# Performance work log

Hardware: AMD Instinct MI355X
Metric: run time of the kernel (lower is better)

The kernel has to match this reference:

```python
import jax, jax.numpy as jnp
import numpy as np

D_MODEL = 1024
N_HEADS = 16
N_KV = 4
HEAD_DIM = 64
R = 256
B, N = 2, 2048


def setup_inputs() -> dict:
    key = jax.random.key(0)
    ks = jax.random.split(key, 5)
    x = jax.random.normal(ks[0], (B, N, D_MODEL), jnp.float32)
    # rotary cos/sin table: (N, HEAD_DIM//2, 2)
    inv = 1.0 / (10000.0 ** (jnp.arange(0, HEAD_DIM, 2, dtype=jnp.float32) / HEAD_DIM))
    ang = jnp.arange(N, dtype=jnp.float32)[:, None] * inv[None, :]
    freqs_cis = jnp.stack([jnp.cos(ang), jnp.sin(ang)], axis=-1)
    s = 0.02
    Wq = jax.random.normal(ks[1], (D_MODEL, N_HEADS * HEAD_DIM), jnp.float32) * s
    Wk = jax.random.normal(ks[2], (D_MODEL, N_KV * HEAD_DIM), jnp.float32) * s
    Wv = jax.random.normal(ks[3], (D_MODEL, N_KV * HEAD_DIM), jnp.float32) * s
    Wo = jax.random.normal(ks[4], (N_HEADS * HEAD_DIM, D_MODEL), jnp.float32) * s
    return dict(x=x, freqs_cis=freqs_cis, Wq=Wq, Wk=Wk, Wv=Wv, Wo=Wo)


def _select_pairs(scores_i, best_b_i, r):
    """Greedy top-r pair selection with unique-b constraint (one batch row)."""
    half = scores_i.shape[0]
    order = jnp.argsort(-scores_i)  # descending by best similarity

    def step(carry, a_local):
        used, count = carry
        b_local = best_b_i[a_local]
        take = jnp.logical_and(jnp.logical_not(used[b_local]), count < r)
        used = used.at[b_local].set(used[b_local] | take)
        count = count + take.astype(jnp.int32)
        return (used, count), (take, a_local.astype(jnp.int32), b_local.astype(jnp.int32))

    (_, count), (takes, a_locs, b_locs) = jax.lax.scan(
        step, (jnp.zeros(half, bool), jnp.int32(0)), order)
    pos = jnp.cumsum(takes.astype(jnp.int32)) - 1
    idx = jnp.where(takes, pos, r)  # dump non-taken into slot r
    sel_a = jnp.zeros(r + 1, jnp.int32).at[idx].set(a_locs)[:r]
    sel_b = jnp.zeros(r + 1, jnp.int32).at[idx].set(b_locs)[:r]
    valid = jnp.arange(r) < count  # pad (if fewer than r unique) with first pair
    sel_a = jnp.where(valid, sel_a, sel_a[0])
    sel_b = jnp.where(valid, sel_b, sel_b[0])
    return sel_a, sel_b


def bipartite_indices(metric, r):
    """Returns (global_a, global_b, keep_idx) for merge/unmerge."""
    Bm, Nm, _ = metric.shape
    a = metric[:, 0::2]  # (B, half, C)
    b = metric[:, 1::2]
    an = a / jnp.maximum(jnp.linalg.norm(a, axis=-1, keepdims=True), 1e-12)
    bn = b / jnp.maximum(jnp.linalg.norm(b, axis=-1, keepdims=True), 1e-12)
    scores = jnp.einsum('bic,bjc->bij', an, bn)  # (B, half, half)
    best_scores = scores.max(axis=2)
    best_b = scores.argmax(axis=2)
    sel_a, sel_b = jax.vmap(lambda s, m: _select_pairs(s, m, r))(best_scores, best_b)
    global_a = 2 * sel_a      # even indices
    global_b = 2 * sel_b + 1  # odd indices
    bidx = jnp.arange(Bm)[:, None]
    keep_mask = jnp.ones((Bm, Nm), bool).at[bidx, global_b].set(False)
    # stable argsort puts kept (False) positions first, in original order
    keep_idx = jnp.argsort(~keep_mask, axis=1)[:, :Nm - r]
    return global_a, global_b, keep_idx


def merge(x, global_a, global_b, keep_idx):
    Bm = x.shape[0]
    bidx = jnp.arange(Bm)[:, None]
    xa = jnp.take_along_axis(x, global_a[..., None], axis=1)
    xb = jnp.take_along_axis(x, global_b[..., None], axis=1)
    x_out = x.at[bidx, global_a].set((xa + xb) * 0.5)
    return jnp.take_along_axis(x_out, keep_idx[..., None], axis=1)


def unmerge(xm, global_a, global_b, keep_idx, n_orig):
    Bm, _, C = xm.shape
    bidx = jnp.arange(Bm)[:, None]
    out = jnp.zeros((Bm, n_orig, C), xm.dtype).at[bidx, keep_idx].set(xm)
    xa = jnp.take_along_axis(out, global_a[..., None], axis=1)
    return out.at[bidx, global_b].set(xa)


def _rope(t, freqs):
    # t: (B, N, H, HD), freqs: (N, HD//2, 2)
    cos = freqs[None, :, None, :, 0]
    sin = freqs[None, :, None, :, 1]
    t1 = t[..., 0::2]
    t2 = t[..., 1::2]
    rot = jnp.stack([t1 * cos - t2 * sin, t1 * sin + t2 * cos], axis=-1)
    return rot.reshape(t.shape)


def _attention(x_m, freqs, Wq, Wk, Wv, Wo):
    Bm, Nm, _ = x_m.shape
    q = (x_m @ Wq).reshape(Bm, Nm, N_HEADS, HEAD_DIM)
    k = (x_m @ Wk).reshape(Bm, Nm, N_KV, HEAD_DIM)
    v = (x_m @ Wv).reshape(Bm, Nm, N_KV, HEAD_DIM)
    q = _rope(q, freqs)
    k = _rope(k, freqs)
    rep = N_HEADS // N_KV
    k = jnp.repeat(k, rep, axis=2)
    v = jnp.repeat(v, rep, axis=2)
    att = jnp.einsum('bqhd,bkhd->bhqk', q, k) / np.sqrt(HEAD_DIM).astype(np.float32)
    w = jax.nn.softmax(att, axis=-1)
    o = jnp.einsum('bhqk,bkhd->bqhd', w, v).reshape(Bm, Nm, N_HEADS * HEAD_DIM)
    return o @ Wo


def reference(x, freqs_cis, Wq, Wk, Wv, Wo):
    n = x.shape[1]
    metric = jax.lax.stop_gradient(x @ Wk)  # k_proj under no_grad
    ga, gb, ki = bipartite_indices(metric, R)
    x_m = merge(x, ga, gb, ki)
    n_merged = x_m.shape[1]
    out_m = _attention(x_m, freqs_cis[:n_merged], Wq, Wk, Wv, Wo)
    return unmerge(out_m, ga, gb, ki, n)
```

## Files before the change

kernel.cpp:

```cpp
#include <hip/hip_runtime.h>
#include <hip/hip_bf16.h>
#include <math.h>

#define BB 2
#define NN 2048
#define DM 1024
#define NH 16
#define NKV 4
#define HD 64
#define RR 256
#define HALF 1024
#define NM 1792
#define NT 28
#define NSPL 2

typedef __bf16 bf16x8 __attribute__((ext_vector_type(8)));
typedef float f32x4 __attribute__((ext_vector_type(4)));

__device__ inline unsigned pk2(float a, float b) {
  union { __bf16 h; unsigned short u; } ua, ub;
  ua.h = (__bf16)a;
  ub.h = (__bf16)b;
  return (unsigned)ua.u | ((unsigned)ub.u << 16);
}

__device__ inline unsigned shu(unsigned v, int s) {
  return (unsigned)__shfl((int)v, s, 64);
}

__global__ __launch_bounds__(256) void gemm_bf16(
    const __bf16* __restrict__ A, const __bf16* __restrict__ Bt,
    float* __restrict__ C, int M, int N, int K) {
  __shared__ __align__(16) __bf16 As[4096];
  __shared__ __align__(16) __bf16 Bs[4096];
  const int bm0 = blockIdx.x * 64;
  const int bn0 = blockIdx.y * 64;
  const int w = threadIdx.x >> 6;
  const int lane = threadIdx.x & 63;
  f32x4 acc[4];
#pragma unroll
  for (int nt = 0; nt < 4; ++nt) acc[nt] = (f32x4){0.f, 0.f, 0.f, 0.f};
  for (int kk = 0; kk < K; kk += 64) {
    __syncthreads();
#pragma unroll
    for (int t2 = threadIdx.x; t2 < 512; t2 += 256) {
      const int blk = t2 >> 7, s = (t2 >> 6) & 1, l = t2 & 63;
      const int kc = kk + s * 32 + ((l >> 4) << 3);
      *(float4*)&As[t2 * 8] =
          *(const float4*)(A + (size_t)(bm0 + blk * 16 + (l & 15)) * K + kc);
      *(float4*)&Bs[t2 * 8] =
          *(const float4*)(Bt + (size_t)(bn0 + blk * 16 + (l & 15)) * K + kc);
    }
    __syncthreads();
#pragma unroll
    for (int s = 0; s < 2; ++s) {
      bf16x8 a = *(const bf16x8*)&As[((w * 2 + s) * 64 + lane) * 8];
#pragma unroll
      for (int nt = 0; nt < 4; ++nt) {
        bf16x8 bfr = *(const bf16x8*)&Bs[((nt * 2 + s) * 64 + lane) * 8];
        acc[nt] =
            __builtin_amdgcn_mfma_f32_16x16x32_bf16(a, bfr, acc[nt], 0, 0, 0);
      }
    }
  }
  const int g = lane >> 4, ml = lane & 15;
#pragma unroll
  for (int nt = 0; nt < 4; ++nt)
#pragma unroll
    for (int r = 0; r < 4; ++r)
      C[(size_t)(bm0 + w * 16 + g * 4 + r) * N + bn0 + nt * 16 + ml] =
          acc[nt][r];
}

__global__ __launch_bounds__(256) void gemm_wo(
    const __bf16* __restrict__ A, const __bf16* __restrict__ Bt,
    const int* __restrict__ keep_idx, const int* __restrict__ dst2,
    float* __restrict__ out, int M, int N, int K) {
  __shared__ __align__(16) __bf16 As[4096];
  __shared__ __align__(16) __bf16 Bs[4096];
  const int bm0 = blockIdx.x * 64;
  const int bn0 = blockIdx.y * 64;
  const int w = threadIdx.x >> 6;
  const int lane = threadIdx.x & 63;
  f32x4 acc[4];
#pragma unroll
  for (int nt = 0; nt < 4; ++nt) acc[nt] = (f32x4){0.f, 0.f, 0.f, 0.f};
  for (int kk = 0; kk < K; kk += 64) {
    __syncthreads();
#pragma unroll
    for (int t2 = threadIdx.x; t2 < 512; t2 += 256) {
      const int blk = t2 >> 7, s = (t2 >> 6) & 1, l = t2 & 63;
      const int kc = kk + s * 32 + ((l >> 4) << 3);
      *(float4*)&As[t2 * 8] =
          *(const float4*)(A + (size_t)(bm0 + blk * 16 + (l & 15)) * K + kc);
      *(float4*)&Bs[t2 * 8] =
          *(const float4*)(Bt + (size_t)(bn0 + blk * 16 + (l & 15)) * K + kc);
    }
    __syncthreads();
#pragma unroll
    for (int s = 0; s < 2; ++s) {
      bf16x8 a = *(const bf16x8*)&As[((w * 2 + s) * 64 + lane) * 8];
#pragma unroll
      for (int nt = 0; nt < 4; ++nt) {
        bf16x8 bfr = *(const bf16x8*)&Bs[((nt * 2 + s) * 64 + lane) * 8];
        acc[nt] =
            __builtin_amdgcn_mfma_f32_16x16x32_bf16(a, bfr, acc[nt], 0, 0, 0);
      }
    }
  }
  const int g = lane >> 4, ml = lane & 15;
#pragma unroll
  for (int r = 0; r < 4; ++r) {
    const int row = bm0 + w * 16 + g * 4 + r;
    const int bb = row / NM, tt = row % NM;
    const int p1 = keep_idx[bb * NM + tt];
    const int p2 = dst2[bb * NM + tt];
#pragma unroll
    for (int nt = 0; nt < 4; ++nt) {
      const int col = bn0 + nt * 16 + ml;
      float v = acc[nt][r];
      out[((size_t)(bb * NN + p1)) * DM + col] = v;
      if (p2 >= 0) out[((size_t)(bb * NN + p2)) * DM + col] = v;
    }
  }
}

__global__ __launch_bounds__(256) void gemm_hiloA(
    const float* __restrict__ A, const __bf16* __restrict__ Bh,
    const __bf16* __restrict__ Bl, float* __restrict__ C0,
    float* __restrict__ C1, int M, int N, int K) {
  __shared__ __align__(16) __bf16 Ah[4096], Al[4096], Bhs[4096], Bls[4096];
  const int z = blockIdx.z;
  float* C = z ? C1 : C0;
  const int kof = z * (K / 2);
  const int bm0 = blockIdx.x * 64;
  const int bn0 = blockIdx.y * 64;
  const int w = threadIdx.x >> 6;
  const int lane = threadIdx.x & 63;
  f32x4 acc[4];
#pragma unroll
  for (int nt = 0; nt < 4; ++nt) acc[nt] = (f32x4){0.f, 0.f, 0.f, 0.f};
  for (int kk = kof; kk < kof + K / 2; kk += 64) {
    __syncthreads();
#pragma unroll
    for (int t2 = threadIdx.x; t2 < 512; t2 += 256) {
      const int blk = t2 >> 7, s = (t2 >> 6) & 1, l = t2 & 63;
      const int row = bm0 + blk * 16 + (l & 15);
      const int rowB = bn0 + blk * 16 + (l & 15);
      const int col = kk + s * 32 + ((l >> 4) << 3);
      {
        float4 f0 = *(const float4*)(A + (size_t)row * K + col);
        float4 f1 = *(const float4*)(A + (size_t)row * K + col + 4);
        float ff[8] = {f0.x, f0.y, f0.z, f0.w, f1.x, f1.y, f1.z, f1.w};
        union { __bf16 h[8]; float4 q; } H, L;
#pragma unroll
        for (int j = 0; j < 8; ++j) {
          __bf16 hh = (__bf16)ff[j];
          H.h[j] = hh;
          L.h[j] = (__bf16)(ff[j] - (float)hh);
        }
        *(float4*)&Ah[t2 * 8] = H.q;
        *(float4*)&Al[t2 * 8] = L.q;
      }
      *(float4*)&Bhs[t2 * 8] = *(const float4*)(Bh + (size_t)rowB * K + col);
      *(float4*)&Bls[t2 * 8] = *(const float4*)(Bl + (size_t)rowB * K + col);
    }
    __syncthreads();
#pragma unroll
    for (int s = 0; s < 2; ++s) {
      bf16x8 ah = *(const bf16x8*)&Ah[((w * 2 + s) * 64 + lane) * 8];
      bf16x8 al = *(const bf16x8*)&Al[((w * 2 + s) * 64 + lane) * 8];
#pragma unroll
      for (int nt = 0; nt < 4; ++nt) {
        bf16x8 bh = *(const bf16x8*)&Bhs[((nt * 2 + s) * 64 + lane) * 8];
        bf16x8 bl = *(const bf16x8*)&Bls[((nt * 2 + s) * 64 + lane) * 8];
        acc[nt] = __builtin_amdgcn_mfma_f32_16x16x32_bf16(al, bh, acc[nt], 0, 0, 0);
        acc[nt] = __builtin_amdgcn_mfma_f32_16x16x32_bf16(ah, bl, acc[nt], 0, 0, 0);
        acc[nt] = __builtin_amdgcn_mfma_f32_16x16x32_bf16(ah, bh, acc[nt], 0, 0, 0);
      }
    }
  }
  const int g = lane >> 4, ml = lane & 15;
#pragma unroll
  for (int nt = 0; nt < 4; ++nt)
#pragma unroll
    for (int r = 0; r < 4; ++r)
      C[(size_t)(bm0 + w * 16 + g * 4 + r) * N + bn0 + nt * 16 + ml] =
          acc[nt][r];
}

__global__ __launch_bounds__(256) void gemm_sc3(
    const __bf16* __restrict__ Ah, const __bf16* __restrict__ Al,
    const __bf16* __restrict__ Bh, const __bf16* __restrict__ Bl,
    float* __restrict__ C) {
  __shared__ __align__(16) __bf16 Ahs[4096], Als[4096], Bhs[4096], Bls[4096];
  const size_t zo = (size_t)blockIdx.z * HALF * 256;
  C += (size_t)blockIdx.z * HALF * HALF;
  const int bm0 = blockIdx.x * 64;
  const int bn0 = blockIdx.y * 64;
  const int w = threadIdx.x >> 6;
  const int lane = threadIdx.x & 63;
  f32x4 acc[4];
#pragma unroll
  for (int nt = 0; nt < 4; ++nt) acc[nt] = (f32x4){0.f, 0.f, 0.f, 0.f};
  for (int kk = 0; kk < 256; kk += 64) {
    __syncthreads();
#pragma unroll
    for (int t2 = threadIdx.x; t2 < 512; t2 += 256) {
      const int blk = t2 >> 7, s = (t2 >> 6) & 1, l = t2 & 63;
      const size_t ra = zo + (size_t)(bm0 + blk * 16 + (l & 15)) * 256;
      const size_t rb = zo + (size_t)(bn0 + blk * 16 + (l & 15)) * 256;
      const int col = kk + s * 32 + ((l >> 4) << 3);
      *(float4*)&Ahs[t2 * 8] = *(const float4*)(Ah + ra + col);
      *(float4*)&Als[t2 * 8] = *(const float4*)(Al + ra + col);
      *(float4*)&Bhs[t2 * 8] = *(const float4*)(Bh + rb + col);
      *(float4*)&Bls[t2 * 8] = *(const float4*)(Bl + rb + col);
    }
    __syncthreads();
#pragma unroll
    for (int s = 0; s < 2; ++s) {
      bf16x8 ah = *(const bf16x8*)&Ahs[((w * 2 + s) * 64 + lane) * 8];
      bf16x8 al = *(const bf16x8*)&Als[((w * 2 + s) * 64 + lane) * 8];
#pragma unroll
      for (int nt = 0; nt < 4; ++nt) {
        bf16x8 bh = *(const bf16x8*)&Bhs[((nt * 2 + s) * 64 + lane) * 8];
        bf16x8 bl = *(const bf16x8*)&Bls[((nt * 2 + s) * 64 + lane) * 8];
        acc[nt] = __builtin_amdgcn_mfma_f32_16x16x32_bf16(al, bh, acc[nt], 0, 0, 0);
        acc[nt] = __builtin_amdgcn_mfma_f32_16x16x32_bf16(ah, bl, acc[nt], 0, 0, 0);
        acc[nt] = __builtin_amdgcn_mfma_f32_16x16x32_bf16(ah, bh, acc[nt], 0, 0, 0);
      }
    }
  }
  const int g = lane >> 4, ml = lane & 15;
#pragma unroll
  for (int nt = 0; nt < 4; ++nt)
#pragma unroll
    for (int r = 0; r < 4; ++r)
      C[(size_t)(bm0 + w * 16 + g * 4 + r) * HALF + bn0 + nt * 16 + ml] =
          acc[nt][r];
}

__global__ __launch_bounds__(256) void transpose_wk(
    const float* __restrict__ W, __bf16* __restrict__ Wh,
    __bf16* __restrict__ Wl) {
  __shared__ float ld[64][65];
  const int k0 = blockIdx.x * 64, n0 = blockIdx.y * 64;
  for (int i = threadIdx.x; i < 1024; i += 256) {
    int r = i >> 4, c4 = i & 15;
    float4 v = *(const float4*)(W + (size_t)(k0 + r) * 256 + n0 + c4 * 4);
    ld[r][c4 * 4 + 0] = v.x;
    ld[r][c4 * 4 + 1] = v.y;
    ld[r][c4 * 4 + 2] = v.z;
    ld[r][c4 * 4 + 3] = v.w;
  }
  __syncthreads();
  for (int i = threadIdx.x; i < 4096; i += 256) {
    int n = i >> 6, k = i & 63;
    float v = ld[k][n];
    __bf16 hh = (__bf16)v;
    Wh[(size_t)(n0 + n) * 1024 + k0 + k] = hh;
    Wl[(size_t)(n0 + n) * 1024 + k0 + k] = (__bf16)(v - (float)hh);
  }
}

__global__ __launch_bounds__(256) void transpose_bf16(
    const float* __restrict__ W, __bf16* __restrict__ Wt, int K, int N) {
  __shared__ float ld[64][65];
  const int k0 = blockIdx.x * 64, n0 = blockIdx.y * 64;
  for (int i = threadIdx.x; i < 1024; i += 256) {
    int r = i >> 4, c4 = i & 15;
    float4 v = *(const float4*)(W + (size_t)(k0 + r) * N + n0 + c4 * 4);
    ld[r][c4 * 4 + 0] = v.x;
    ld[r][c4 * 4 + 1] = v.y;
    ld[r][c4 * 4 + 2] = v.z;
    ld[r][c4 * 4 + 3] = v.w;
  }
  __syncthreads();
  for (int i = threadIdx.x; i < 4096; i += 256) {
    int n = i >> 6, k = i & 63;
    Wt[(size_t)(n0 + n) * K + k0 + k] = (__bf16)ld[k][n];
  }
}

__global__ __launch_bounds__(256) void normalize_split(
    const float* __restrict__ m0, const float* __restrict__ m1,
    __bf16* __restrict__ anh, __bf16* __restrict__ anl,
    __bf16* __restrict__ bnh, __bf16* __restrict__ bnl) {
  const int row = blockIdx.x;
  const int b = row >> 11;
  const int r = row & 2047;
  const int t = threadIdx.x;
  float v = m0[(size_t)row * 256 + t] + m1[(size_t)row * 256 + t];
  float ss = v * v;
#pragma unroll
  for (int o = 32; o > 0; o >>= 1) ss += __shfl_xor(ss, o, 64);
  __shared__ float wsum[4];
  if ((t & 63) == 0) wsum[t >> 6] = ss;
  __syncthreads();
  float tot = wsum[0] + wsum[1] + wsum[2] + wsum[3];
  float inv = 1.f / fmaxf(sqrtf(tot), 1e-12f);
  float nv = v * inv;
  __bf16 hh = (__bf16)nv;
  __bf16 ll = (__bf16)(nv - (float)hh);
  size_t o = ((size_t)b * HALF + (r >> 1)) * 256 + t;
  if (r & 1) {
    bnh[o] = hh;
    bnl[o] = ll;
  } else {
    anh[o] = hh;
    anl[o] = ll;
  }
}

__global__ __launch_bounds__(256) void argmax_rows(
    const float* __restrict__ scores, float* __restrict__ best_s,
    int* __restrict__ best_b) {
  const int rid = blockIdx.x * 4 + (threadIdx.x >> 6);
  const int lane = threadIdx.x & 63;
  const float4* row = (const float4*)(scores + (size_t)rid * 1024);
  float bv = -3.4e38f;
  int bj = 0;
#pragma unroll
  for (int p = 0; p < 4; ++p) {
    float4 f = row[p * 64 + lane];
    int j0 = (p * 64 + lane) * 4;
    if (f.x > bv) { bv = f.x; bj = j0; }
    if (f.y > bv) { bv = f.y; bj = j0 + 1; }
    if (f.z > bv) { bv = f.z; bj = j0 + 2; }
    if (f.w > bv) { bv = f.w; bj = j0 + 3; }
  }
#pragma unroll
  for (int off = 1; off < 64; off <<= 1) {
    float vo = __shfl_xor(bv, off, 64);
    int jo = __shfl_xor(bj, off, 64);
    if (vo > bv || (vo == bv && jo < bj)) { bv = vo; bj = jo; }
  }
  if (lane == 0) {
    best_s[rid] = bv;
    best_b[rid] = bj;
  }
}

__global__ __launch_bounds__(512) void sort_desc(const float* __restrict__ best_s,
                                                 int* __restrict__ order) {
  const int b = blockIdx.x;
  __shared__ float sv[1024];
  __shared__ int si[1024];
  for (int i = threadIdx.x; i < 1024; i += 512) {
    sv[i] = best_s[b * HALF + i];
    si[i] = i;
  }
  __syncthreads();
  for (int k = 2; k <= 1024; k <<= 1) {
    for (int j = k >> 1; j > 0; j >>= 1) {
      for (int t = threadIdx.x; t < 1024; t += 512) {
        int ixj = t ^ j;
        if (ixj > t) {
          bool dir = ((t & k) == 0);
          float va = sv[t], vb = sv[ixj];
          int ia = si[t], ib = si[ixj];
          bool before = (vb > va) || (vb == va && ib < ia);
          if (before == dir) {
            sv[t] = vb; sv[ixj] = va;
            si[t] = ib; si[ixj] = ia;
          }
        }
      }
      __syncthreads();
    }
  }
  for (int i = threadIdx.x; i < 1024; i += 512) order[b * HALF + i] = si[i];
}

__global__ __launch_bounds__(256) void select_and_index(
    const int* __restrict__ best_b, const int* __restrict__ order,
    int* __restrict__ keep_idx, int* __restrict__ partner,
    int* __restrict__ dst2) {
  const int b = blockIdx.x;
  __shared__ int rankA[HALF];
  __shared__ int minrank[HALF];
  __shared__ int taken[HALF];
  __shared__ int sel_a[RR], sel_b[RR];
  __shared__ int removed[NN];
  __shared__ int src_row[NN];
  __shared__ int tsum[256];
  const int t = threadIdx.x;

  for (int i = t; i < HALF; i += 256) { minrank[i] = 0x7fffffff; taken[i] = 0; }
  for (int i = t; i < NN; i += 256) {
    removed[i] = 0;
    partner[b * NN + i] = -1;
  }
  for (int i = t; i < NM; i += 256) dst2[b * NM + i] = -1;
  __syncthreads();
  int ord[4];
#pragma unroll
  for (int q = 0; q < 4; ++q) {
    int step = t * 4 + q;
    ord[q] = order[b * HALF + step];
    rankA[ord[q]] = step;
  }
  __syncthreads();
#pragma unroll
  for (int q = 0; q < 4; ++q) {
    int a = t * 4 + q;
    atomicMin(&minrank[best_b[b * HALF + a]], rankA[a]);
  }
  __syncthreads();
  for (int i = t; i < HALF; i += 256) {
    int mr = minrank[i];
    if (mr != 0x7fffffff) taken[mr] = 1;
  }
  __syncthreads();
  int c[4];
  int mysum = 0;
#pragma unroll
  for (int q = 0; q < 4; ++q) { c[q] = taken[t * 4 + q]; mysum += c[q]; }
  tsum[t] = mysum;
  __syncthreads();
  for (int off = 1; off < 256; off <<= 1) {
    int v = (t >= off) ? tsum[t - off] : 0;
    __syncthreads();
    tsum[t] += v;
    __syncthreads();
  }
  int run = tsum[t] - mysum;
#pragma unroll
  for (int q = 0; q < 4; ++q) {
    if (c[q] && run < RR) {
      int a = ord[q];
      sel_a[run] = 2 * a;
      sel_b[run] = 2 * best_b[b * HALF + a] + 1;
    }
    run += c[q];
  }
  __syncthreads();
  const int cnt = min(tsum[255], RR);
  if (t >= cnt) { sel_a[t] = sel_a[0]; sel_b[t] = sel_b[0]; }
  __syncthreads();
  {
    int ga = sel_a[t], gb = sel_b[t];
    removed[gb] = 1;
    partner[b * NN + ga] = gb;
  }
  __syncthreads();
  int myc = 0;
#pragma unroll
  for (int q = 0; q < 8; ++q) myc += !removed[8 * t + q];
  tsum[t] = myc;
  __syncthreads();
  for (int off = 1; off < 256; off <<= 1) {
    int v = (t >= off) ? tsum[t - off] : 0;
    __syncthreads();
    tsum[t] += v;
    __syncthreads();
  }
  int pos = tsum[t] - myc;
#pragma unroll
  for (int q = 0; q < 8; ++q) {
    int p = 8 * t + q;
    int sr = -1;
    if (!removed[p]) {
      if (pos < NM) {
        keep_idx[b * NM + pos] = p;
        sr = pos;
      }
      ++pos;
    }
    src_row[p] = sr;
  }
  __syncthreads();
  {
    int sr = src_row[sel_a[t]];
    dst2[b * NM + sr] = sel_b[t];
  }
}

__global__ __launch_bounds__(256) void merge_kernel(
    const float* __restrict__ x, const int* __restrict__ keep_idx,
    const int* __restrict__ partner, __bf16* __restrict__ x_mb) {
  const int mrow = blockIdx.x;
  const int b = mrow / NM;
  const int t = mrow % NM;
  const int p = keep_idx[b * NM + t];
  const int pp = partner[b * NN + p];
  const float4* src =
      reinterpret_cast<const float4*>(x + ((size_t)b * NN + p) * DM);
  float4 val = src[threadIdx.x];
  if (pp >= 0) {
    const float4* s2 =
        reinterpret_cast<const float4*>(x + ((size_t)b * NN + pp) * DM);
    float4 v2 = s2[threadIdx.x];
    val.x = 0.5f * (val.x + v2.x);
    val.y = 0.5f * (val.y + v2.y);
    val.z = 0.5f * (val.z + v2.z);
    val.w = 0.5f * (val.w + v2.w);
  }
  union { __bf16 h[4]; uint2 u; } U;
  U.h[0] = (__bf16)val.x;
  U.h[1] = (__bf16)val.y;
  U.h[2] = (__bf16)val.z;
  U.h[3] = (__bf16)val.w;
  ((uint2*)(x_mb + (size_t)mrow * DM))[threadIdx.x] = U.u;
}

__global__ __launch_bounds__(256) void rope_fused(
    const float* __restrict__ qb, const float* __restrict__ kb,
    const float* __restrict__ fc, __bf16* __restrict__ qbh,
    __bf16* __restrict__ kbh) {
  const int row = blockIdx.x;
  const int t = row % NM;
  const int b = row / NM;
  for (int idx = threadIdx.x; idx < 640; idx += 256) {
    int u = idx & 31;
    float c = fc[(t * 32 + u) * 2];
    float s = fc[(t * 32 + u) * 2 + 1];
    if (idx < 512) {
      int h = idx >> 5;
      const float* p = qb + (size_t)row * DM + h * 64 + 2 * u;
      float x1 = p[0], x2 = p[1];
      __bf16* d = qbh + ((size_t)(b * NH + h) * NM + t) * 64 + 2 * u;
      d[0] = (__bf16)((x1 * c - x2 * s) * 0.125f);
      d[1] = (__bf16)((x1 * s + x2 * c) * 0.125f);
    } else {
      int h = (idx - 512) >> 5;
      const float* p = kb + (size_t)row * 256 + h * 64 + 2 * u;
      float x1 = p[0], x2 = p[1];
      __bf16* d = kbh + ((size_t)(b * NKV + h) * NM + t) * 64 + 2 * u;
      d[0] = (__bf16)(x1 * c - x2 * s);
      d[1] = (__bf16)(x1 * s + x2 * c);
    }
  }
}

__global__ __launch_bounds__(256) void v_repack(const float* __restrict__ vb,
                                                __bf16* __restrict__ vtb) {
  __shared__ float ld[64][65];
  int bid = blockIdx.x;
  const int kt = bid % (NM / 64); bid /= (NM / 64);
  const int kvh = bid % NKV;
  const int b = bid / NKV;
  const int j0 = kt * 64;
  for (int t2 = threadIdx.x; t2 < 1024; t2 += 256) {
    int key = t2 >> 4, c4 = t2 & 15;
    float4 v4 = *reinterpret_cast<const float4*>(
        vb + (((size_t)(b * NM + j0 + key)) * NKV + kvh) * 64 + c4 * 4);
    ld[key][c4 * 4 + 0] = v4.x;
    ld[key][c4 * 4 + 1] = v4.y;
    ld[key][c4 * 4 + 2] = v4.z;
    ld[key][c4 * 4 + 3] = v4.w;
  }
  __syncthreads();
  const int dim = threadIdx.x >> 2, kc = threadIdx.x & 3;
  __bf16* out = vtb + ((size_t)(b * NKV + kvh) * 64 + dim) * NM + j0 + kc * 16;
#pragma unroll
  for (int kk = 0; kk < 16; ++kk) out[kk] = (__bf16)ld[kc * 16 + kk][dim];
}

__global__ __launch_bounds__(512) void attn_mfma(
    const __bf16* __restrict__ qbh,
    const __bf16* __restrict__ kbh,
    const __bf16* __restrict__ vtb,
    float* __restrict__ pl, __bf16* __restrict__ pacc) {
  __shared__ __align__(16) __bf16 Ks[4096];
  __shared__ __align__(16) __bf16 Vs[4096];
  int bid = blockIdx.x;
  const int qt2 = bid % (NM / 32); bid /= (NM / 32);
  const int split = bid % NSPL; bid /= NSPL;
  const int kvh = bid % NKV;
  const int b = bid / NKV;
  const int w = threadIdx.x >> 6;
  const int lane = threadIdx.x & 63;
  const int h = kvh * 4 + (w & 3);
  const int qt = qt2 * 32 + (w >> 2) * 16;
  const int g = lane >> 4;
  const int ml = lane & 15;

  const __bf16* qrow = qbh + ((size_t)(b * NH + h) * NM + qt + ml) * 64;
  bf16x8 qa0 = *reinterpret_cast<const bf16x8*>(qrow + g * 8);
  bf16x8 qa1 = *reinterpret_cast<const bf16x8*>(qrow + 32 + g * 8);

  f32x4 acc[4];
#pragma unroll
  for (int mt = 0; mt < 4; ++mt) acc[mt] = (f32x4){0.f, 0.f, 0.f, 0.f};
  float lsum = 0.f;

  const __bf16* kp = kbh + (size_t)(b * NKV + kvh) * NM * 64;
  const __bf16* vp = vtb + (size_t)(b * NKV + kvh) * 64 * NM;
  const int src0 = ((lane >> 4) & 1) * 32 + ml;
  const int src1 = src0 + 16;
  const int sel = g >> 1;

  const int jt0 = split * (NT / NSPL);
  for (int jt = jt0; jt < jt0 + NT / NSPL; ++jt) {
    __syncthreads();
    {
      const int t2 = threadIdx.x;
      const int blk = t2 >> 7, s = (t2 >> 6) & 1, l = t2 & 63;
      *(float4*)&Ks[t2 * 8] = *(const float4*)(
          kp + (size_t)(jt * 64 + blk * 16 + (l & 15)) * 64 + s * 32 +
          ((l >> 4) << 3));
      *(float4*)&Vs[t2 * 8] = *(const float4*)(
          vp + (size_t)(blk * 16 + (l & 15)) * NM + jt * 64 + s * 32 +
          ((l >> 4) << 3));
    }
    __syncthreads();
    f32x4 S[4];
#pragma unroll
    for (int nt = 0; nt < 4; ++nt) {
      bf16x8 k0 = *(const bf16x8*)&Ks[(nt * 128 + lane) * 8];
      bf16x8 k1 = *(const bf16x8*)&Ks[(nt * 128 + 64 + lane) * 8];
      f32x4 s4 = (f32x4){0.f, 0.f, 0.f, 0.f};
      s4 = __builtin_amdgcn_mfma_f32_16x16x32_bf16(k0, qa0, s4, 0, 0, 0);
      s4 = __builtin_amdgcn_mfma_f32_16x16x32_bf16(k1, qa1, s4, 0, 0, 0);
      S[nt] = s4;
    }
    float p[4][4];
#pragma unroll
    for (int nt = 0; nt < 4; ++nt)
#pragma unroll
      for (int r = 0; r < 4; ++r) {
        p[nt][r] = __expf(S[nt][r]);
        lsum += p[nt][r];
      }
    unsigned pk[4][2];
#pragma unroll
    for (int nt = 0; nt < 4; ++nt) {
      pk[nt][0] = pk2(p[nt][0], p[nt][1]);
      pk[nt][1] = pk2(p[nt][2], p[nt][3]);
    }
    unsigned A00 = shu(pk[0][0], src0), A01 = shu(pk[0][1], src0);
    unsigned A10 = shu(pk[1][0], src0), A11 = shu(pk[1][1], src0);
    unsigned B00 = shu(pk[0][0], src1), B01 = shu(pk[0][1], src1);
    unsigned B10 = shu(pk[1][0], src1), B11 = shu(pk[1][1], src1);
    unsigned C00 = shu(pk[2][0], src0), C01 = shu(pk[2][1], src0);
    unsigned C10 = shu(pk[3][0], src0), C11 = shu(pk[3][1], src0);
    unsigned D00 = shu(pk[2][0], src1), D01 = shu(pk[2][1], src1);
    unsigned D10 = shu(pk[3][0], src1), D11 = shu(pk[3][1], src1);
    union { uint4 u; bf16x8 v; } P0, P1;
    P0.u.x = sel ? A10 : A00; P0.u.y = sel ? A11 : A01;
    P0.u.z = sel ? B10 : B00; P0.u.w = sel ? B11 : B01;
    P1.u.x = sel ? C10 : C00; P1.u.y = sel ? C11 : C01;
    P1.u.z = sel ? D10 : D00; P1.u.w = sel ? D11 : D01;
#pragma unroll
    for (int mt = 0; mt < 4; ++mt) {
      bf16x8 v0 = *(const bf16x8*)&Vs[(mt * 128 + lane) * 8];
      bf16x8 v1 = *(const bf16x8*)&Vs[(mt * 128 + 64 + lane) * 8];
      acc[mt] = __builtin_amdgcn_mfma_f32_16x16x32_bf16(v0, P0.v, acc[mt], 0, 0, 0);
      acc[mt] = __builtin_amdgcn_mfma_f32_16x16x32_bf16(v1, P1.v, acc[mt], 0, 0, 0);
    }
  }
  lsum += __shfl_xor(lsum, 16, 64);
  lsum += __shfl_xor(lsum, 32, 64);
  const size_t row = (size_t)(b * NH + h) * NM + qt + ml;
  if (g == 0) pl[row * NSPL + split] = lsum;
  __bf16* pa = pacc + (row * NSPL + split) * 64;
#pragma unroll
  for (int mt = 0; mt < 4; ++mt) {
    uint2 u;
    u.x = pk2(acc[mt][0], acc[mt][1]);
    u.y = pk2(acc[mt][2], acc[mt][3]);
    *reinterpret_cast<uint2*>(pa + mt * 16 + g * 4) = u;
  }
}

__global__ __launch_bounds__(256) void attn_combine(
    const float* __restrict__ pl, const __bf16* __restrict__ pacc,
    __bf16* __restrict__ attn_ob) {
  const size_t rid = (size_t)blockIdx.x * 4 + (threadIdx.x >> 6);
  const int d = threadIdx.x & 63;
  float a0 = (float)pacc[(rid * NSPL + 0) * 64 + d];
  float a1 = (float)pacc[(rid * NSPL + 1) * 64 + d];
  float den = pl[rid * NSPL + 0] + pl[rid * NSPL + 1];
  float o = (a0 + a1) / den;
  const int q = (int)(rid % NM);
  const int h = (int)((rid / NM) % NH);
  const int b = (int)(rid / ((size_t)NM * NH));
  attn_ob[((size_t)(b * NM + q)) * DM + h * 64 + d] = (__bf16)o;
}

extern "C" void kernel_launch(void* const* d_in, const int* in_sizes, int n_in,
                              void* d_out, int out_size, void* d_ws,
                              size_t ws_size, hipStream_t stream) {
  const float* x = (const float*)d_in[0];
  const float* fc = (const float*)d_in[1];
  const float* Wq = (const float*)d_in[2];
  const float* Wk = (const float*)d_in[3];
  const float* Wv = (const float*)d_in[4];
  const float* Wo = (const float*)d_in[5];
  float* out = (float*)d_out;

  char* ws = (char*)d_ws;
  size_t off = 0;
  auto alloc = [&](size_t bytes) {
    void* p = ws + off;
    off += (bytes + 255) & ~(size_t)255;
    return p;
  };
  float* metric0 = (float*)alloc((size_t)BB * NN * 256 * 4);
  float* metric1 = (float*)alloc((size_t)BB * NN * 256 * 4);
  float* best_s = (float*)alloc((size_t)BB * HALF * 4);
  int* best_b = (int*)alloc((size_t)BB * HALF * 4);
  int* order = (int*)alloc((size_t)BB * HALF * 4);
  int* keep_idx = (int*)alloc((size_t)BB * NM * 4);
  int* partner = (int*)alloc((size_t)BB * NN * 4);
  int* dst2 = (int*)alloc((size_t)BB * NM * 4);
  char* bigreg = (char*)alloc((size_t)18 * 1024 * 1024);
  float* scores = (float*)bigreg;
  __bf16* anh = (__bf16*)(bigreg + (size_t)9500 * 1024);
  __bf16* anl = (__bf16*)(bigreg + (size_t)10600 * 1024);
  __bf16* bnh = (__bf16*)(bigreg + (size_t)11700 * 1024);
  __bf16* bnl = (__bf16*)(bigreg + (size_t)12800 * 1024);
  float* qb = (float*)bigreg;
  __bf16* pacc = (__bf16*)bigreg;
  __bf16* x_mb = (__bf16*)alloc((size_t)BB * NM * DM * 2);
  float* kb = (float*)alloc((size_t)BB * NM * NKV * HD * 4);
  float* vb = (float*)alloc((size_t)BB * NM * NKV * HD * 4);
  __bf16* qbh = (__bf16*)alloc((size_t)BB * NH * NM * 64 * 2);
  __bf16* kbh = (__bf16*)alloc((size_t)BB * NKV * NM * 64 * 2);
  __bf16* vtb = (__bf16*)alloc((size_t)BB * NKV * 64 * NM * 2);
  __bf16* attn_ob = (__bf16*)alloc((size_t)BB * NM * DM * 2);
  float* pl = (float*)alloc((size_t)BB * NH * NM * NSPL * 4);
  __bf16* Wkth = (__bf16*)alloc((size_t)256 * DM * 2);
  __bf16* Wktl = (__bf16*)alloc((size_t)256 * DM * 2);
  __bf16* Wqt = (__bf16*)alloc((size_t)DM * DM * 2);
  __bf16* Wvt = (__bf16*)alloc((size_t)256 * DM * 2);
  __bf16* Wot = (__bf16*)alloc((size_t)DM * DM * 2);

  transpose_wk<<<dim3(16, 4), 256, 0, stream>>>(Wk, Wkth, Wktl);
  transpose_bf16<<<dim3(16, 16), 256, 0, stream>>>(Wq, Wqt, DM, DM);
  transpose_bf16<<<dim3(16, 4), 256, 0, stream>>>(Wv, Wvt, DM, 256);
  transpose_bf16<<<dim3(16, 16), 256, 0, stream>>>(Wo, Wot, DM, DM);
  gemm_hiloA<<<dim3(64, 4, 2), 256, 0, stream>>>(x, Wkth, Wktl, metric0,
                                                 metric1, BB * NN, 256, DM);
  normalize_split<<<BB * NN, 256, 0, stream>>>(metric0, metric1, anh, anl, bnh,
                                               bnl);
  gemm_sc3<<<dim3(16, 16, 2), 256, 0, stream>>>(anh, anl, bnh, bnl, scores);
  argmax_rows<<<(BB * HALF) / 4, 256, 0, stream>>>(scores, best_s, best_b);
  sort_desc<<<BB, 512, 0, stream>>>(best_s, order);
  select_and_index<<<BB, 256, 0, stream>>>(best_b, order, keep_idx, partner,
                                           dst2);
  merge_kernel<<<BB * NM, 256, 0, stream>>>(x, keep_idx, partner, x_mb);
  gemm_bf16<<<dim3(56, 16), 256, 0, stream>>>(x_mb, Wqt, qb, BB * NM, DM, DM);
  gemm_bf16<<<dim3(56, 4), 256, 0, stream>>>(x_mb, Wkth, kb, BB * NM, 256, DM);
  gemm_bf16<<<dim3(56, 4), 256, 0, stream>>>(x_mb, Wvt, vb, BB * NM, 256, DM);
  rope_fused<<<BB * NM, 256, 0, stream>>>(qb, kb, fc, qbh, kbh);
  v_repack<<<BB * NKV * (NM / 64), 256, 0, stream>>>(vb, vtb);
  attn_mfma<<<BB * NKV * NSPL * (NM / 32), 512, 0, stream>>>(qbh, kbh, vtb, pl,
                                                             pacc);
  attn_combine<<<(BB * NH * NM) / 4, 256, 0, stream>>>(pl, pacc, attn_ob);
  gemm_wo<<<dim3(56, 16), 256, 0, stream>>>(attn_ob, Wot, keep_idx, dst2, out,
                                            BB * NM, DM, DM);
}
```

Measured before the change: 339.4 us.

## Fuse QKV projections, fold argmax into score GEMM, batch weight transposes

```diff
diff --git a/kernel.cpp b/kernel.cpp
--- a/kernel.cpp
+++ b/kernel.cpp
@@ -12,7 +12,7 @@
 #define HALF 1024
 #define NM 1792
 #define NT 28
-#define NSPL 2
+#define NSPL 4
 
 typedef __bf16 bf16x8 __attribute__((ext_vector_type(8)));
 typedef float f32x4 __attribute__((ext_vector_type(4)));
@@ -125,11 +125,11 @@
   }
 }
 
-__global__ __launch_bounds__(256) void gemm_hiloA(
-    const float* __restrict__ A, const __bf16* __restrict__ Bh,
-    const __bf16* __restrict__ Bl, float* __restrict__ C0,
-    float* __restrict__ C1, int M, int N, int K) {
-  __shared__ __align__(16) __bf16 Ah[4096], Al[4096], Bhs[4096], Bls[4096];
+__global__ __launch_bounds__(256) void gemm3t(
+    const __bf16* __restrict__ Ah, const __bf16* __restrict__ Al,
+    const __bf16* __restrict__ Bh, const __bf16* __restrict__ Bl,
+    float* __restrict__ C0, float* __restrict__ C1, int M, int N, int K) {
+  __shared__ __align__(16) __bf16 Ahs[4096], Als[4096], Bhs[4096], Bls[4096];
   const int z = blockIdx.z;
   float* C = z ? C1 : C0;
   const int kof = z * (K / 2);
@@ -145,31 +145,19 @@
 #pragma unroll
     for (int t2 = threadIdx.x; t2 < 512; t2 += 256) {
       const int blk = t2 >> 7, s = (t2 >> 6) & 1, l = t2 & 63;
-      const int row = bm0 + blk * 16 + (l & 15);
-      const int rowB = bn0 + blk * 16 + (l & 15);
+      const size_t ra = (size_t)(bm0 + blk * 16 + (l & 15)) * K;
+      const size_t rb = (size_t)(bn0 + blk * 16 + (l & 15)) * K;
       const int col = kk + s * 32 + ((l >> 4) << 3);
-      {
-        float4 f0 = *(const float4*)(A + (size_t)row * K + col);
-        float4 f1 = *(const float4*)(A + (size_t)row * K + col + 4);
-        float ff[8] = {f0.x, f0.y, f0.z, f0.w, f1.x, f1.y, f1.z, f1.w};
-        union { __bf16 h[8]; float4 q; } H, L;
-#pragma unroll
-        for (int j = 0; j < 8; ++j) {
-          __bf16 hh = (__bf16)ff[j];
-          H.h[j] = hh;
-          L.h[j] = (__bf16)(ff[j] - (float)hh);
-        }
-        *(float4*)&Ah[t2 * 8] = H.q;
-        *(float4*)&Al[t2 * 8] = L.q;
-      }
-      *(float4*)&Bhs[t2 * 8] = *(const float4*)(Bh + (size_t)rowB * K + col);
-      *(float4*)&Bls[t2 * 8] = *(const float4*)(Bl + (size_t)rowB * K + col);
+      *(float4*)&Ahs[t2 * 8] = *(const float4*)(Ah + ra + col);
+      *(float4*)&Als[t2 * 8] = *(const float4*)(Al + ra + col);
+      *(float4*)&Bhs[t2 * 8] = *(const float4*)(Bh + rb + col);
+      *(float4*)&Bls[t2 * 8] = *(const float4*)(Bl + rb + col);
     }
     __syncthreads();
 #pragma unroll
     for (int s = 0; s < 2; ++s) {
-      bf16x8 ah = *(const bf16x8*)&Ah[((w * 2 + s) * 64 + lane) * 8];
-      bf16x8 al = *(const bf16x8*)&Al[((w * 2 + s) * 64 + lane) * 8];
+      bf16x8 ah = *(const bf16x8*)&Ahs[((w * 2 + s) * 64 + lane) * 8];
+      bf16x8 al = *(const bf16x8*)&Als[((w * 2 + s) * 64 + lane) * 8];
 #pragma unroll
       for (int nt = 0; nt < 4; ++nt) {
         bf16x8 bh = *(const bf16x8*)&Bhs[((nt * 2 + s) * 64 + lane) * 8];
@@ -189,13 +177,12 @@
           acc[nt][r];
 }
 
-__global__ __launch_bounds__(256) void gemm_sc3(
+__global__ __launch_bounds__(256) void gemm_scam(
     const __bf16* __restrict__ Ah, const __bf16* __restrict__ Al,
     const __bf16* __restrict__ Bh, const __bf16* __restrict__ Bl,
-    float* __restrict__ C) {
+    float* __restrict__ sval, int* __restrict__ sidx) {
   __shared__ __align__(16) __bf16 Ahs[4096], Als[4096], Bhs[4096], Bls[4096];
   const size_t zo = (size_t)blockIdx.z * HALF * 256;
-  C += (size_t)blockIdx.z * HALF * HALF;
   const int bm0 = blockIdx.x * 64;
   const int bn0 = blockIdx.y * 64;
   const int w = threadIdx.x >> 6;
@@ -233,21 +220,97 @@
   }
   const int g = lane >> 4, ml = lane & 15;
 #pragma unroll
-  for (int nt = 0; nt < 4; ++nt)
-#pragma unroll
-    for (int r = 0; r < 4; ++r)
-      C[(size_t)(bm0 + w * 16 + g * 4 + r) * HALF + bn0 + nt * 16 + ml] =
-          acc[nt][r];
-}
-
-__global__ __launch_bounds__(256) void transpose_wk(
-    const float* __restrict__ W, __bf16* __restrict__ Wh,
-    __bf16* __restrict__ Wl) {
+  for (int r = 0; r < 4; ++r) {
+    float bv = acc[0][r];
+    int bc = bn0 + ml;
+#pragma unroll
+    for (int nt = 1; nt < 4; ++nt) {
+      float v = acc[nt][r];
+      int c = bn0 + nt * 16 + ml;
+      if (v > bv) { bv = v; bc = c; }
+    }
+#pragma unroll
+    for (int off = 1; off < 16; off <<= 1) {
+      float vo = __shfl_xor(bv, off, 64);
+      int co = __shfl_xor(bc, off, 64);
+      if (vo > bv || (vo == bv && co < bc)) { bv = vo; bc = co; }
+    }
+    if (ml == 0) {
+      const int row = bm0 + w * 16 + g * 4 + r;
+      const size_t o = ((size_t)blockIdx.z * HALF + row) * 16 + (bn0 >> 6);
+      sval[o] = bv;
+      sidx[o] = bc;
+    }
+  }
+}
+
+__global__ __launch_bounds__(256) void argmax_reduce(
+    const float* __restrict__ sval, const int* __restrict__ sidx,
+    float* __restrict__ best_s, int* __restrict__ best_b) {
+  const int lane = threadIdx.x & 63;
+  const int e = lane & 15;
+  const int rid = blockIdx.x * 16 + (threadIdx.x >> 6) * 4 + (lane >> 4);
+  float bv = sval[rid * 16 + e];
+  int bc = sidx[rid * 16 + e];
+#pragma unroll
+  for (int off = 1; off < 16; off <<= 1) {
+    float vo = __shfl_xor(bv, off, 64);
+    int co = __shfl_xor(bc, off, 64);
+    if (vo > bv || (vo == bv && co < bc)) { bv = vo; bc = co; }
+  }
+  if (e == 0) {
+    best_s[rid] = bv;
+    best_b[rid] = bc;
+  }
+}
+
+__global__ __launch_bounds__(256) void hilo_split(const float* __restrict__ x,
+                                                  __bf16* __restrict__ xh,
+                                                  __bf16* __restrict__ xl) {
+  const int i = blockIdx.x * 256 + threadIdx.x;
+  float4 v = ((const float4*)x)[i];
+  float f[4] = {v.x, v.y, v.z, v.w};
+  union { __bf16 h[4]; uint2 u; } H, L;
+#pragma unroll
+  for (int j = 0; j < 4; ++j) {
+    __bf16 hh = (__bf16)f[j];
+    H.h[j] = hh;
+    L.h[j] = (__bf16)(f[j] - (float)hh);
+  }
+  ((uint2*)xh)[i] = H.u;
+  ((uint2*)xl)[i] = L.u;
+}
+
+__global__ __launch_bounds__(256) void transpose_all(
+    const float* __restrict__ Wq, const float* __restrict__ Wk,
+    const float* __restrict__ Wv, const float* __restrict__ Wo,
+    __bf16* __restrict__ Wqkvt, __bf16* __restrict__ Wktl,
+    __bf16* __restrict__ Wot) {
   __shared__ float ld[64][65];
-  const int k0 = blockIdx.x * 64, n0 = blockIdx.y * 64;
+  const int z = blockIdx.x;
+  const float* src;
+  __bf16* dsth;
+  __bf16* dstl = nullptr;
+  int N, k0, n0, rowoff;
+  if (z < 256) {
+    src = Wq; N = 1024; k0 = (z >> 4) << 6; n0 = (z & 15) << 6;
+    dsth = Wqkvt; rowoff = 0;
+  } else if (z < 320) {
+    int zz = z - 256;
+    src = Wk; N = 256; k0 = (zz >> 2) << 6; n0 = (zz & 3) << 6;
+    dsth = Wqkvt; rowoff = 1024; dstl = Wktl;
+  } else if (z < 384) {
+    int zz = z - 320;
+    src = Wv; N = 256; k0 = (zz >> 2) << 6; n0 = (zz & 3) << 6;
+    dsth = Wqkvt; rowoff = 1280;
+  } else {
+    int zz = z - 384;
+    src = Wo; N = 1024; k0 = (zz >> 4) << 6; n0 = (zz & 15) << 6;
+    dsth = Wot; rowoff = 0;
+  }
   for (int i = threadIdx.x; i < 1024; i += 256) {
     int r = i >> 4, c4 = i & 15;
-    float4 v = *(const float4*)(W + (size_t)(k0 + r) * 256 + n0 + c4 * 4);
+    float4 v = *(const float4*)(src + (size_t)(k0 + r) * N + n0 + c4 * 4);
     ld[r][c4 * 4 + 0] = v.x;
     ld[r][c4 * 4 + 1] = v.y;
     ld[r][c4 * 4 + 2] = v.z;
@@ -258,27 +321,9 @@
     int n = i >> 6, k = i & 63;
     float v = ld[k][n];
     __bf16 hh = (__bf16)v;
-    Wh[(size_t)(n0 + n) * 1024 + k0 + k] = hh;
-    Wl[(size_t)(n0 + n) * 1024 + k0 + k] = (__bf16)(v - (float)hh);
-  }
-}
-
-__global__ __launch_bounds__(256) void transpose_bf16(
-    const float* __restrict__ W, __bf16* __restrict__ Wt, int K, int N) {
-  __shared__ float ld[64][65];
-  const int k0 = blockIdx.x * 64, n0 = blockIdx.y * 64;
-  for (int i = threadIdx.x; i < 1024; i += 256) {
-    int r = i >> 4, c4 = i & 15;
-    float4 v = *(const float4*)(W + (size_t)(k0 + r) * N + n0 + c4 * 4);
-    ld[r][c4 * 4 + 0] = v.x;
-    ld[r][c4 * 4 + 1] = v.y;
-    ld[r][c4 * 4 + 2] = v.z;
-    ld[r][c4 * 4 + 3] = v.w;
-  }
-  __syncthreads();
-  for (int i = threadIdx.x; i < 4096; i += 256) {
-    int n = i >> 6, k = i & 63;
-    Wt[(size_t)(n0 + n) * K + k0 + k] = (__bf16)ld[k][n];
+    dsth[(size_t)(rowoff + n0 + n) * 1024 + k0 + k] = hh;
+    if (dstl)
+      dstl[(size_t)(n0 + n) * 1024 + k0 + k] = (__bf16)(v - (float)hh);
   }
 }
 
@@ -309,35 +354,6 @@
   } else {
     anh[o] = hh;
     anl[o] = ll;
-  }
-}
-
-__global__ __launch_bounds__(256) void argmax_rows(
-    const float* __restrict__ scores, float* __restrict__ best_s,
-    int* __restrict__ best_b) {
-  const int rid = blockIdx.x * 4 + (threadIdx.x >> 6);
-  const int lane = threadIdx.x & 63;
-  const float4* row = (const float4*)(scores + (size_t)rid * 1024);
-  float bv = -3.4e38f;
-  int bj = 0;
-#pragma unroll
-  for (int p = 0; p < 4; ++p) {
-    float4 f = row[p * 64 + lane];
-    int j0 = (p * 64 + lane) * 4;
-    if (f.x > bv) { bv = f.x; bj = j0; }
-    if (f.y > bv) { bv = f.y; bj = j0 + 1; }
-    if (f.z > bv) { bv = f.z; bj = j0 + 2; }
-    if (f.w > bv) { bv = f.w; bj = j0 + 3; }
-  }
-#pragma unroll
-  for (int off = 1; off < 64; off <<= 1) {
-    float vo = __shfl_xor(bv, off, 64);
-    int jo = __shfl_xor(bj, off, 64);
-    if (vo > bv || (vo == bv && jo < bj)) { bv = vo; bj = jo; }
-  }
-  if (lane == 0) {
-    best_s[rid] = bv;
-    best_b[rid] = bj;
   }
 }
 
@@ -505,9 +521,8 @@
 }
 
 __global__ __launch_bounds__(256) void rope_fused(
-    const float* __restrict__ qb, const float* __restrict__ kb,
-    const float* __restrict__ fc, __bf16* __restrict__ qbh,
-    __bf16* __restrict__ kbh) {
+    const float* __restrict__ qkv, const float* __restrict__ fc,
+    __bf16* __restrict__ qbh, __bf16* __restrict__ kbh) {
   const int row = blockIdx.x;
   const int t = row % NM;
   const int b = row / NM;
@@ -517,14 +532,14 @@
     float s = fc[(t * 32 + u) * 2 + 1];
     if (idx < 512) {
       int h = idx >> 5;
-      const float* p = qb + (size_t)row * DM + h * 64 + 2 * u;
+      const float* p = qkv + (size_t)row * 1536 + h * 64 + 2 * u;
       float x1 = p[0], x2 = p[1];
       __bf16* d = qbh + ((size_t)(b * NH + h) * NM + t) * 64 + 2 * u;
       d[0] = (__bf16)((x1 * c - x2 * s) * 0.125f);
       d[1] = (__bf16)((x1 * s + x2 * c) * 0.125f);
     } else {
       int h = (idx - 512) >> 5;
-      const float* p = kb + (size_t)row * 256 + h * 64 + 2 * u;
+      const float* p = qkv + (size_t)row * 1536 + 1024 + h * 64 + 2 * u;
       float x1 = p[0], x2 = p[1];
       __bf16* d = kbh + ((size_t)(b * NKV + h) * NM + t) * 64 + 2 * u;
       d[0] = (__bf16)(x1 * c - x2 * s);
@@ -533,7 +548,7 @@
   }
 }
 
-__global__ __launch_bounds__(256) void v_repack(const float* __restrict__ vb,
+__global__ __launch_bounds__(256) void v_repack(const float* __restrict__ qkv,
                                                 __bf16* __restrict__ vtb) {
   __shared__ float ld[64][65];
   int bid = blockIdx.x;
@@ -544,7 +559,7 @@
   for (int t2 = threadIdx.x; t2 < 1024; t2 += 256) {
     int key = t2 >> 4, c4 = t2 & 15;
     float4 v4 = *reinterpret_cast<const float4*>(
-        vb + (((size_t)(b * NM + j0 + key)) * NKV + kvh) * 64 + c4 * 4);
+        qkv + (size_t)(b * NM + j0 + key) * 1536 + 1280 + kvh * 64 + c4 * 4);
     ld[key][c4 * 4 + 0] = v4.x;
     ld[key][c4 * 4 + 1] = v4.y;
     ld[key][c4 * 4 + 2] = v4.z;
@@ -558,10 +573,9 @@
 }
 
 __global__ __launch_bounds__(512) void attn_mfma(
-    const __bf16* __restrict__ qbh,
-    const __bf16* __restrict__ kbh,
-    const __bf16* __restrict__ vtb,
-    float* __restrict__ pl, __bf16* __restrict__ pacc) {
+    const __bf16* __restrict__ qbh, const __bf16* __restrict__ kbh,
+    const __bf16* __restrict__ vtb, float* __restrict__ pl,
+    __bf16* __restrict__ pacc) {
   __shared__ __align__(16) __bf16 Ks[4096];
   __shared__ __align__(16) __bf16 Vs[4096];
   int bid = blockIdx.x;
@@ -669,10 +683,13 @@
     __bf16* __restrict__ attn_ob) {
   const size_t rid = (size_t)blockIdx.x * 4 + (threadIdx.x >> 6);
   const int d = threadIdx.x & 63;
-  float a0 = (float)pacc[(rid * NSPL + 0) * 64 + d];
-  float a1 = (float)pacc[(rid * NSPL + 1) * 64 + d];
-  float den = pl[rid * NSPL + 0] + pl[rid * NSPL + 1];
-  float o = (a0 + a1) / den;
+  float num = 0.f, den = 0.f;
+#pragma unroll
+  for (int s = 0; s < NSPL; ++s) {
+    num += (float)pacc[(rid * NSPL + s) * 64 + d];
+    den += pl[rid * NSPL + s];
+  }
+  float o = num / den;
   const int q = (int)(rid % NM);
   const int h = (int)((rid / NM) % NH);
   const int b = (int)(rid / ((size_t)NM * NH));
@@ -705,47 +722,46 @@
   int* keep_idx = (int*)alloc((size_t)BB * NM * 4);
   int* partner = (int*)alloc((size_t)BB * NN * 4);
   int* dst2 = (int*)alloc((size_t)BB * NM * 4);
-  char* bigreg = (char*)alloc((size_t)18 * 1024 * 1024);
-  float* scores = (float*)bigreg;
-  __bf16* anh = (__bf16*)(bigreg + (size_t)9500 * 1024);
-  __bf16* anl = (__bf16*)(bigreg + (size_t)10600 * 1024);
-  __bf16* bnh = (__bf16*)(bigreg + (size_t)11700 * 1024);
-  __bf16* bnl = (__bf16*)(bigreg + (size_t)12800 * 1024);
-  float* qb = (float*)bigreg;
+  float* sval = (float*)alloc((size_t)BB * HALF * 16 * 4);
+  int* sidx = (int*)alloc((size_t)BB * HALF * 16 * 4);
+  char* bigreg = (char*)alloc((size_t)30 * 1024 * 1024);
+  __bf16* xh = (__bf16*)bigreg;
+  __bf16* xl = (__bf16*)(bigreg + (size_t)8704 * 1024);
+  __bf16* anh = (__bf16*)bigreg;
+  __bf16* anl = (__bf16*)(bigreg + (size_t)1100 * 1024);
+  __bf16* bnh = (__bf16*)(bigreg + (size_t)2200 * 1024);
+  __bf16* bnl = (__bf16*)(bigreg + (size_t)3300 * 1024);
+  float* qkv = (float*)bigreg;
   __bf16* pacc = (__bf16*)bigreg;
   __bf16* x_mb = (__bf16*)alloc((size_t)BB * NM * DM * 2);
-  float* kb = (float*)alloc((size_t)BB * NM * NKV * HD * 4);
-  float* vb = (float*)alloc((size_t)BB * NM * NKV * HD * 4);
   __bf16* qbh = (__bf16*)alloc((size_t)BB * NH * NM * 64 * 2);
   __bf16* kbh = (__bf16*)alloc((size_t)BB * NKV * NM * 64 * 2);
   __bf16* vtb = (__bf16*)alloc((size_t)BB * NKV * 64 * NM * 2);
   __bf16* attn_ob = (__bf16*)alloc((size_t)BB * NM * DM * 2);
   float* pl = (float*)alloc((size_t)BB * NH * NM * NSPL * 4);
-  __bf16* Wkth = (__bf16*)alloc((size_t)256 * DM * 2);
+  __bf16* Wqkvt = (__bf16*)alloc((size_t)1536 * DM * 2);
   __bf16* Wktl = (__bf16*)alloc((size_t)256 * DM * 2);
-  __bf16* Wqt = (__bf16*)alloc((size_t)DM * DM * 2);
-  __bf16* Wvt = (__bf16*)alloc((size_t)256 * DM * 2);
   __bf16* Wot = (__bf16*)alloc((size_t)DM * DM * 2);
-
-  transpose_wk<<<dim3(16, 4), 256, 0, stream>>>(Wk, Wkth, Wktl);
-  transpose_bf16<<<dim3(16, 16), 256, 0, stream>>>(Wq, Wqt, DM, DM);
-  transpose_bf16<<<dim3(16, 4), 256, 0, stream>>>(Wv, Wvt, DM, 256);
-  transpose_bf16<<<dim3(16, 16), 256, 0, stream>>>(Wo, Wot, DM, DM);
-  gemm_hiloA<<<dim3(64, 4, 2), 256, 0, stream>>>(x, Wkth, Wktl, metric0,
-                                                 metric1, BB * NN, 256, DM);
+  const __bf16* Wkth = Wqkvt + (size_t)1024 * 1024;
+
+  transpose_all<<<640, 256, 0, stream>>>(Wq, Wk, Wv, Wo, Wqkvt, Wktl, Wot);
+  hilo_split<<<(BB * NN * DM / 4) / 256, 256, 0, stream>>>(x, xh, xl);
+  gemm3t<<<dim3(64, 4, 2), 256, 0, stream>>>(xh, xl, Wkth, Wktl, metric0,
+                                             metric1, BB * NN, 256, DM);
   normalize_split<<<BB * NN, 256, 0, stream>>>(metric0, metric1, anh, anl, bnh,
                                                bnl);
-  gemm_sc3<<<dim3(16, 16, 2), 256, 0, stream>>>(anh, anl, bnh, bnl, scores);
-  argmax_rows<<<(BB * HALF) / 4, 256, 0, stream>>>(scores, best_s, best_b);
+  gemm_scam<<<dim3(16, 16, 2), 256, 0, stream>>>(anh, anl, bnh, bnl, sval,
+                                                 sidx);
+  argmax_reduce<<<(BB * HALF) / 16, 256, 0, stream>>>(sval, sidx, best_s,
+                                                      best_b);
   sort_desc<<<BB, 512, 0, stream>>>(best_s, order);
   select_and_index<<<BB, 256, 0, stream>>>(best_b, order, keep_idx, partner,
                                            dst2);
   merge_kernel<<<BB * NM, 256, 0, stream>>>(x, keep_idx, partner, x_mb);
-  gemm_bf16<<<dim3(56, 16), 256, 0, stream>>>(x_mb, Wqt, qb, BB * NM, DM, DM);
-  gemm_bf16<<<dim3(56, 4), 256, 0, stream>>>(x_mb, Wkth, kb, BB * NM, 256, DM);
-  gemm_bf16<<<dim3(56, 4), 256, 0, stream>>>(x_mb, Wvt, vb, BB * NM, 256, DM);
-  rope_fused<<<BB * NM, 256, 0, stream>>>(qb, kb, fc, qbh, kbh);
-  v_repack<<<BB * NKV * (NM / 64), 256, 0, stream>>>(vb, vtb);
+  gemm_bf16<<<dim3(56, 24), 256, 0, stream>>>(x_mb, Wqkvt, qkv, BB * NM, 1536,
+                                              DM);
+  rope_fused<<<BB * NM, 256, 0, stream>>>(qkv, fc, qbh, kbh);
+  v_repack<<<BB * NKV * (NM / 64), 256, 0, stream>>>(qkv, vtb);
   attn_mfma<<<BB * NKV * NSPL * (NM / 32), 512, 0, stream>>>(qbh, kbh, vtb, pl,
                                                              pacc);
   attn_combine<<<(BB * NH * NM) / 4, 256, 0, stream>>>(pl, pacc, attn_ob);
```

After: 306.6 us. 9.7% less time.
